# Performance work log

Measured on AMD Instinct MI355X. Metric: run time of the kernel, lower is better.

The kernel has to match this reference:

```python
import jax, jax.numpy as jnp
import numpy as np

N_Q, N_T, D, C = 4096, 8192, 512, 16
SIGMA = 2.0


def setup_inputs() -> dict:
    key = jax.random.key(0)
    k1, k2, k3 = jax.random.split(key, 3)
    X = jax.random.normal(k1, (N_Q, D), dtype=jnp.float32)
    X_train = jax.random.normal(k2, (N_T, D), dtype=jnp.float32)
    y = jax.random.randint(k3, (N_T,), 0, C, dtype=jnp.int32)
    sigma = jnp.float32(SIGMA)
    return {"X": X, "X_train": X_train, "y": y, "sigma": sigma}


def reference(X, X_train, y, sigma):
    xx = jnp.sum(X * X, axis=1, keepdims=True)              # [N_q, 1]
    tt = jnp.sum(X_train * X_train, axis=1)                 # [N_t]
    cross = jnp.einsum('qd,td->qt', X, X_train)             # [N_q, N_t]
    dist2 = jnp.maximum(xx + tt[None, :] - 2.0 * cross, 0.0)
    pattern = jnp.exp(-dist2 / (2.0 * sigma ** 2))          # Gaussian RBF kernel [N_q, N_t]
    # per-class segment sum over training patterns (replaces per-class Python loop)
    summation = jax.ops.segment_sum(pattern.T, y, num_segments=C).T  # [N_q, C]
    summation = summation / jnp.sum(summation, axis=1, keepdims=True)
    return jnp.argmax(summation, axis=1)
```

## Files before the change

kernel.cpp:

```cpp
#include <hip/hip_runtime.h>


#define NQ 4096
#define NT 8192
#define DD 512
#define NC 16
#define LN_FLT_MIN -87.336544750402f
#define SCREEN_T 730.0f

typedef __attribute__((ext_vector_type(4))) int   v4i;
typedef __attribute__((ext_vector_type(8))) int   v8i;
typedef __attribute__((ext_vector_type(16))) float f32x16;

__global__ __launch_bounds__(256) void prep_k(const float* __restrict__ X,
                                              const float* __restrict__ XT,
                                              unsigned char* __restrict__ fXp,
                                              unsigned char* __restrict__ fTp,
                                              float* __restrict__ xx,
                                              float* __restrict__ tt,
                                              float* __restrict__ classacc) {
  const int lane = threadIdx.x & 63;
  const int row  = blockIdx.x * 4 + (threadIdx.x >> 6);
  const float* src; unsigned char* dst; float* nrm; int r;
  if (row < NT) { r = row; src = XT + (size_t)r * DD; dst = fTp; nrm = tt + r; }
  else { r = row - NT; src = X + (size_t)r * DD; dst = fXp; nrm = xx + r; }
  const float4* s4 = (const float4*)src;
  const float4 a = s4[lane * 2], b = s4[lane * 2 + 1];
  int w0 = __builtin_amdgcn_cvt_pk_fp8_f32(a.x, a.y, 0, false);
  w0     = __builtin_amdgcn_cvt_pk_fp8_f32(a.z, a.w, w0, true);
  int w1 = __builtin_amdgcn_cvt_pk_fp8_f32(b.x, b.y, 0, false);
  w1     = __builtin_amdgcn_cvt_pk_fp8_f32(b.z, b.w, w1, true);
  int2 o; o.x = w0; o.y = w1;
  const int l = (r & 31) + 32 * ((lane >> 2) & 1);
  const size_t dest = ((size_t)(r >> 5) * 8 + (lane >> 3)) * 2048
                    + ((lane >> 1) & 1) * 1024 + l * 16 + (lane & 1) * 8;
  *(int2*)(dst + dest) = o;
  float acc = a.x*a.x + a.y*a.y + a.z*a.z + a.w*a.w
            + b.x*b.x + b.y*b.y + b.z*b.z + b.w*b.w;
  #pragma unroll
  for (int off = 32; off; off >>= 1) acc += __shfl_down(acc, off, 64);
  if (lane == 0) *nrm = acc;
  if (blockIdx.x < 64) {
    float4 z = {0.f, 0.f, 0.f, 0.f};
    ((float4*)classacc)[blockIdx.x * 256 + threadIdx.x] = z;
  }
}

#define MFMA(A, B, C) __builtin_amdgcn_mfma_scale_f32_32x32x64_f8f6f4( \
    (A), (B), (C), 0, 0, 0, 127, 0, 127)

static __device__ __forceinline__ v8i ld32(const unsigned char* p) {
  v4i lo = *(const v4i*)p;
  v4i hi = *(const v4i*)(p + 1024);
  return __builtin_shufflevector(lo, hi, 0, 1, 2, 3, 4, 5, 6, 7);
}

__global__ __launch_bounds__(512) void pnn_mfma(const unsigned char* __restrict__ fXp,
                                                const unsigned char* __restrict__ fTp,
                                                const float* __restrict__ Xf,
                                                const float* __restrict__ Tf,
                                                const int* __restrict__ y,
                                                const float* __restrict__ sigp,
                                                const float* __restrict__ xx,
                                                const float* __restrict__ tt,
                                                float* __restrict__ classacc) {
  const int tid  = threadIdx.x;
  const int wid  = tid >> 6, lane = tid & 63;
  const int la   = lane & 31, lb = lane >> 5;
  const int wr   = wid >> 2, wc = wid & 3;

  const int bid = blockIdx.x;
  const int xcd = bid & 7, cc = bid >> 3;
  const int qt  = (xcd & 1) * 16 + (cc >> 3);
  const int tn  = (xcd >> 1) * 8 + (cc & 7);
  const int wq  = qt * 128 + wr * 64;
  const int wt  = tn * 256 + wc * 64;

  const unsigned char* pa = fXp + ((size_t)(wq >> 5) * 8) * 2048 + lane * 16;
  const unsigned char* pb = fTp + ((size_t)(wt >> 5) * 8) * 2048 + lane * 16;

  f32x16 acc00 = (f32x16)(0.f), acc01 = (f32x16)(0.f);
  f32x16 acc10 = (f32x16)(0.f), acc11 = (f32x16)(0.f);

  v8i A0[2], A1[2], B0[2], B1[2];

#define LOADK(s, kt) { \
    A0[s] = ld32(pa + (kt) * 2048); \
    A1[s] = ld32(pa + 16384 + (kt) * 2048); \
    B0[s] = ld32(pb + (kt) * 2048); \
    B1[s] = ld32(pb + 16384 + (kt) * 2048); }

  LOADK(0, 0)
  LOADK(1, 1)
  #pragma unroll
  for (int kt = 0; kt < 8; ++kt) {
    const int s = kt & 1;
    acc00 = MFMA(A0[s], B0[s], acc00);
    acc01 = MFMA(A0[s], B1[s], acc01);
    acc10 = MFMA(A1[s], B0[s], acc10);
    acc11 = MFMA(A1[s], B1[s], acc11);
    if (kt < 6) LOADK(s, kt + 2)
  }
#undef LOADK

  const float sg = sigp[0];
  const float inv2s2 = 1.0f / (2.0f * sg * sg);
  float tnorm[2]; int tcls[2];
  #pragma unroll
  for (int nt = 0; nt < 2; ++nt) {
    const int t = wt + nt * 32 + la;
    tnorm[nt] = tt[t]; tcls[nt] = y[t];
  }

#define EPIL(ACC, mt, nt) { \
    _Pragma("unroll") \
    for (int reg = 0; reg < 16; ++reg) { \
      const int q = wq + (mt) * 32 + (reg & 3) + 8 * (reg >> 2) + 4 * lb; \
      const float xq = xx[q]; \
      const float d2 = xq + tnorm[(nt)] - 2.0f * (ACC)[reg]; \
      if (__builtin_expect(d2 < SCREEN_T, 0)) { \
        const int t = wt + (nt) * 32 + la; \
        const float4* xp = (const float4*)(Xf + (size_t)q * DD); \
        const float4* tp = (const float4*)(Tf + (size_t)t * DD); \
        float s0 = 0.f, s1 = 0.f, s2 = 0.f, s3 = 0.f; \
        for (int d = 0; d < DD / 4; ++d) { \
          const float4 xv = xp[d], tv = tp[d]; \
          s0 = fmaf(xv.x, tv.x, s0); s1 = fmaf(xv.y, tv.y, s1); \
          s2 = fmaf(xv.z, tv.z, s2); s3 = fmaf(xv.w, tv.w, s3); \
        } \
        const float dot = (s0 + s1) + (s2 + s3); \
        const float dd2 = fmaxf(xq + tnorm[(nt)] - 2.0f * dot, 0.f); \
        const float arg = -dd2 * inv2s2; \
        if (arg >= LN_FLT_MIN)             \
          atomicAdd(&classacc[q * NC + tcls[(nt)]], expf(arg)); \
      } \
    } }

  EPIL(acc00, 0, 0)
  EPIL(acc01, 0, 1)
  EPIL(acc10, 1, 0)
  EPIL(acc11, 1, 1)
#undef EPIL
}

__global__ __launch_bounds__(256) void argmax_k(const float* __restrict__ classacc,
                                                float* __restrict__ out) {
  const int q = blockIdx.x * 256 + threadIdx.x;
  float sc[NC];
  #pragma unroll
  for (int c4 = 0; c4 < 4; ++c4) {
    const float4 v = ((const float4*)(classacc + (size_t)q * NC))[c4];
    sc[c4*4+0] = v.x; sc[c4*4+1] = v.y; sc[c4*4+2] = v.z; sc[c4*4+3] = v.w;
  }
  float rowsum = 0.f;
  #pragma unroll
  for (int c = 0; c < NC; ++c) rowsum += sc[c];
  int best = 0; float bv = sc[0];
  #pragma unroll
  for (int c = 1; c < NC; ++c)
    if (sc[c] > bv) { bv = sc[c]; best = c; }
  out[q] = (rowsum > 0.f) ? (float)best : 0.0f;
}

extern "C" void kernel_launch(void* const* d_in, const int* in_sizes, int n_in,
                              void* d_out, int out_size, void* d_ws, size_t ws_size,
                              hipStream_t stream) {
  const float* X  = (const float*)d_in[0];
  const float* XT = (const float*)d_in[1];
  const int*   y  = (const int*)d_in[2];
  const float* sg = (const float*)d_in[3];
  float* out = (float*)d_out;

  char* wsp = (char*)d_ws;
  unsigned char* fXp = (unsigned char*)wsp;
  unsigned char* fTp = fXp + (size_t)NQ * DD;
  float* tt       = (float*)(wsp + 8u * 1024u * 1024u);
  float* xx       = tt + NT;
  float* classacc = xx + NQ;

  prep_k<<<(NQ + NT) / 4, 256, 0, stream>>>(X, XT, fXp, fTp, xx, tt, classacc);
  pnn_mfma<<<1024, 512, 0, stream>>>(fXp, fTp, X, XT, y, sg, xx, tt, classacc);
  argmax_k<<<NQ / 256, 256, 0, stream>>>(classacc, out);
}
```

Measured before the change: 50.85 us.

## Stage FP8 GEMM operand tiles through LDS with async global_load_lds double buffering

Each warp used to load its A/B fragments straight from global memory into registers, with a two-deep register prefetch. Now the block cooperatively copies each K-slice of the shared 128x256 tile into LDS with global_load_lds, double-buffers it, and waits on vmcnt plus barriers before warps read their fragments from LDS. This removes duplicate global loads of operands shared across warps. It also remaps blocks to tiles per XCD for L2 locality and raises MFMA issue priority. The cost is a barrier at every K step and added LDS traffic.

```diff
diff --git a/kernel.cpp b/kernel.cpp
--- a/kernel.cpp
+++ b/kernel.cpp
@@ -48,8 +48,16 @@
 
 #define MFMA(A, B, C) __builtin_amdgcn_mfma_scale_f32_32x32x64_f8f6f4( \
     (A), (B), (C), 0, 0, 0, 127, 0, 127)
-
-static __device__ __forceinline__ v8i ld32(const unsigned char* p) {
+#define BAR() __builtin_amdgcn_s_barrier()
+#define WAITV(N) asm volatile("s_waitcnt vmcnt(" #N ")" ::: "memory")
+
+static __device__ __forceinline__ void gll(const unsigned char* src, char* dst) {
+  __builtin_amdgcn_global_load_lds(
+      (const __attribute__((address_space(1))) unsigned int*)src,
+      (__attribute__((address_space(3))) unsigned int*)dst, 16, 0, 0);
+}
+
+static __device__ __forceinline__ v8i ld32(const char* p) {
   v4i lo = *(const v4i*)p;
   v4i hi = *(const v4i*)(p + 1024);
   return __builtin_shufflevector(lo, hi, 0, 1, 2, 3, 4, 5, 6, 7);
@@ -64,6 +72,7 @@
                                                 const float* __restrict__ xx,
                                                 const float* __restrict__ tt,
                                                 float* __restrict__ classacc) {
+  __shared__ char lds[49152];
   const int tid  = threadIdx.x;
   const int wid  = tid >> 6, lane = tid & 63;
   const int la   = lane & 31, lb = lane >> 5;
@@ -71,38 +80,55 @@
 
   const int bid = blockIdx.x;
   const int xcd = bid & 7, cc = bid >> 3;
-  const int qt  = (xcd & 1) * 16 + (cc >> 3);
-  const int tn  = (xcd >> 1) * 8 + (cc & 7);
-  const int wq  = qt * 128 + wr * 64;
-  const int wt  = tn * 256 + wc * 64;
-
-  const unsigned char* pa = fXp + ((size_t)(wq >> 5) * 8) * 2048 + lane * 16;
-  const unsigned char* pb = fTp + ((size_t)(wt >> 5) * 8) * 2048 + lane * 16;
+  const int qt  = (xcd & 3) * 8 + (cc >> 4);
+  const int tn  = (xcd >> 2) * 16 + (cc & 15);
+  const int qbase = qt * 128, tbase = tn * 256;
+  const int qrt0 = qbase >> 5;
+  const int trt0 = tbase >> 5;
+
+  const int sc = tid >> 7;
+  const int si = (tid & 127) * 16;
+
+#define STAGE(kt, Ab, Bb) { \
+    gll(fXp + ((size_t)(qrt0 + sc) * 8 + (kt)) * 2048 + si, (Ab) + sc * 2048 + si); \
+    gll(fTp + ((size_t)(trt0 + sc) * 8 + (kt)) * 2048 + si, (Bb) + sc * 2048 + si); \
+    gll(fTp + ((size_t)(trt0 + sc + 4) * 8 + (kt)) * 2048 + si, (Bb) + (sc + 4) * 2048 + si); }
+
+  char* const A0 = lds;
+  char* const A1 = lds + 8192;
+  char* const B0 = lds + 16384;
+  char* const B1 = lds + 32768;
 
   f32x16 acc00 = (f32x16)(0.f), acc01 = (f32x16)(0.f);
   f32x16 acc10 = (f32x16)(0.f), acc11 = (f32x16)(0.f);
 
-  v8i A0[2], A1[2], B0[2], B1[2];
-
-#define LOADK(s, kt) { \
-    A0[s] = ld32(pa + (kt) * 2048); \
-    A1[s] = ld32(pa + 16384 + (kt) * 2048); \
-    B0[s] = ld32(pb + (kt) * 2048); \
-    B1[s] = ld32(pb + 16384 + (kt) * 2048); }
-
-  LOADK(0, 0)
-  LOADK(1, 1)
+  STAGE(0, A0, B0)
+
   #pragma unroll
   for (int kt = 0; kt < 8; ++kt) {
-    const int s = kt & 1;
-    acc00 = MFMA(A0[s], B0[s], acc00);
-    acc01 = MFMA(A0[s], B1[s], acc01);
-    acc10 = MFMA(A1[s], B0[s], acc10);
-    acc11 = MFMA(A1[s], B1[s], acc11);
-    if (kt < 6) LOADK(s, kt + 2)
-  }
-#undef LOADK
-
+    char* const Ac = (kt & 1) ? A1 : A0;
+    char* const Bc = (kt & 1) ? B1 : B0;
+    char* const An = (kt & 1) ? A0 : A1;
+    char* const Bn = (kt & 1) ? B0 : B1;
+    if (kt < 7) { STAGE(kt + 1, An, Bn) }
+    if (kt < 7) { WAITV(3); } else { WAITV(0); }
+    BAR();
+    const v8i a0 = ld32(Ac + (wr * 2 + 0) * 2048 + lane * 16);
+    const v8i a1 = ld32(Ac + (wr * 2 + 1) * 2048 + lane * 16);
+    const v8i b0 = ld32(Bc + (wc * 2 + 0) * 2048 + lane * 16);
+    const v8i b1 = ld32(Bc + (wc * 2 + 1) * 2048 + lane * 16);
+    __builtin_amdgcn_s_setprio(1);
+    acc00 = MFMA(a0, b0, acc00);
+    acc01 = MFMA(a0, b1, acc01);
+    acc10 = MFMA(a1, b0, acc10);
+    acc11 = MFMA(a1, b1, acc11);
+    __builtin_amdgcn_s_setprio(0);
+    if (kt < 7) BAR();
+  }
+#undef STAGE
+
+  const int wq = qbase + wr * 64;
+  const int wt = tbase + wc * 64;
   const float sg = sigp[0];
   const float inv2s2 = 1.0f / (2.0f * sg * sg);
   float tnorm[2]; int tcls[2];
```

New measurement: 48.03 us. -5.5%, faster.

## Restructure FP8 GEMM into persistent LDS-staged blocks with triple-buffered async loads

Applied to the files above, without the earlier changes.

The distance GEMM kernel moves from 1024 blocks of 512 threads, each loading its operands straight from global memory into registers, to 256 blocks of 1024 threads. Each block owns 256 queries and a 512-wide training strip and streams A and B tiles into a three-slot LDS ring via global_load_lds, with waitcnt and barrier synchronisation. Query and training norms and labels are cached in LDS, and the screening test is rewritten as a single compare against precomputed half-norms. The epilogue runs every four stages over 128 training columns and then resets the accumulators. This aims to reuse operand tiles across waves and overlap loads with MFMA, at the cost of about 149 KB of LDS per block, one block per CU, and more barrier overhead.

```diff
diff --git a/kernel.cpp b/kernel.cpp
--- a/kernel.cpp
+++ b/kernel.cpp
@@ -48,99 +48,129 @@
 
 #define MFMA(A, B, C) __builtin_amdgcn_mfma_scale_f32_32x32x64_f8f6f4( \
     (A), (B), (C), 0, 0, 0, 127, 0, 127)
-
-static __device__ __forceinline__ v8i ld32(const unsigned char* p) {
+#define BAR() __builtin_amdgcn_s_barrier()
+#define SBAR() __builtin_amdgcn_sched_barrier(0)
+#define WAITV(N) asm volatile("s_waitcnt vmcnt(" #N ")" ::: "memory")
+
+static __device__ __forceinline__ void gll(const void* src, char* dst) {
+  __builtin_amdgcn_global_load_lds(
+      (const __attribute__((address_space(1))) unsigned int*)src,
+      (__attribute__((address_space(3))) unsigned int*)dst, 16, 0, 0);
+}
+
+static __device__ __forceinline__ v8i ld32(const char* p) {
   v4i lo = *(const v4i*)p;
   v4i hi = *(const v4i*)(p + 1024);
   return __builtin_shufflevector(lo, hi, 0, 1, 2, 3, 4, 5, 6, 7);
 }
 
-__global__ __launch_bounds__(512) void pnn_mfma(const unsigned char* __restrict__ fXp,
-                                                const unsigned char* __restrict__ fTp,
-                                                const float* __restrict__ Xf,
-                                                const float* __restrict__ Tf,
-                                                const int* __restrict__ y,
-                                                const float* __restrict__ sigp,
-                                                const float* __restrict__ xx,
-                                                const float* __restrict__ tt,
-                                                float* __restrict__ classacc) {
+__global__ __launch_bounds__(1024) void pnn_mfma(const unsigned char* __restrict__ fXp,
+                                                 const unsigned char* __restrict__ fTp,
+                                                 const float* __restrict__ Xf,
+                                                 const float* __restrict__ Tf,
+                                                 const int* __restrict__ y,
+                                                 const float* __restrict__ sigp,
+                                                 const float* __restrict__ xx,
+                                                 const float* __restrict__ tt,
+                                                 float* __restrict__ classacc) {
+  extern __shared__ char lds[];
+  char*  const Aring = lds;
+  char*  const Bring = lds + 98304;
+  float* const hxs   = (float*)(lds + 147456);
+  float* const tts   = (float*)(lds + 148480);
+  int*   const ycl   = (int*)  (lds + 150528);
+
   const int tid  = threadIdx.x;
-  const int wid  = tid >> 6, lane = tid & 63;
+  const int w    = tid >> 6, lane = tid & 63;
   const int la   = lane & 31, lb = lane >> 5;
-  const int wr   = wid >> 2, wc = wid & 3;
-
-  const int bid = blockIdx.x;
-  const int xcd = bid & 7, cc = bid >> 3;
-  const int qt  = (xcd & 1) * 16 + (cc >> 3);
-  const int tn  = (xcd >> 1) * 8 + (cc & 7);
-  const int wq  = qt * 128 + wr * 64;
-  const int wt  = tn * 256 + wc * 64;
-
-  const unsigned char* pa = fXp + ((size_t)(wq >> 5) * 8) * 2048 + lane * 16;
-  const unsigned char* pb = fTp + ((size_t)(wt >> 5) * 8) * 2048 + lane * 16;
-
-  f32x16 acc00 = (f32x16)(0.f), acc01 = (f32x16)(0.f);
-  f32x16 acc10 = (f32x16)(0.f), acc11 = (f32x16)(0.f);
-
-  v8i A0[2], A1[2], B0[2], B1[2];
-
-#define LOADK(s, kt) { \
-    A0[s] = ld32(pa + (kt) * 2048); \
-    A1[s] = ld32(pa + 16384 + (kt) * 2048); \
-    B0[s] = ld32(pb + (kt) * 2048); \
-    B1[s] = ld32(pb + 16384 + (kt) * 2048); }
-
-  LOADK(0, 0)
-  LOADK(1, 1)
-  #pragma unroll
-  for (int kt = 0; kt < 8; ++kt) {
-    const int s = kt & 1;
-    acc00 = MFMA(A0[s], B0[s], acc00);
-    acc01 = MFMA(A0[s], B1[s], acc01);
-    acc10 = MFMA(A1[s], B0[s], acc10);
-    acc11 = MFMA(A1[s], B1[s], acc11);
-    if (kt < 6) LOADK(s, kt + 2)
-  }
-#undef LOADK
+  const int wr   = w >> 2, wc = w & 3;
+
+  const int bid   = blockIdx.x;
+  const int strip = bid & 15;
+  const int qt    = bid >> 4;
+  const int qbase = qt * 256;
+  const int qrt   = qbase >> 5;
+  const int trt   = strip * 16;
 
   const float sg = sigp[0];
   const float inv2s2 = 1.0f / (2.0f * sg * sg);
-  float tnorm[2]; int tcls[2];
-  #pragma unroll
-  for (int nt = 0; nt < 2; ++nt) {
-    const int t = wt + nt * 32 + la;
-    tnorm[nt] = tt[t]; tcls[nt] = y[t];
-  }
-
-#define EPIL(ACC, mt, nt) { \
+
+#define STAGE(s) { \
+    char* As = Aring + ((s) % 3) * 32768; \
+    char* Bs = Bring + ((s) % 3) * 16384; \
     _Pragma("unroll") \
-    for (int reg = 0; reg < 16; ++reg) { \
-      const int q = wq + (mt) * 32 + (reg & 3) + 8 * (reg >> 2) + 4 * lb; \
-      const float xq = xx[q]; \
-      const float d2 = xq + tnorm[(nt)] - 2.0f * (ACC)[reg]; \
-      if (__builtin_expect(d2 < SCREEN_T, 0)) { \
-        const int t = wt + (nt) * 32 + la; \
-        const float4* xp = (const float4*)(Xf + (size_t)q * DD); \
-        const float4* tp = (const float4*)(Tf + (size_t)t * DD); \
-        float s0 = 0.f, s1 = 0.f, s2 = 0.f, s3 = 0.f; \
-        for (int d = 0; d < DD / 4; ++d) { \
-          const float4 xv = xp[d], tv = tp[d]; \
-          s0 = fmaf(xv.x, tv.x, s0); s1 = fmaf(xv.y, tv.y, s1); \
-          s2 = fmaf(xv.z, tv.z, s2); s3 = fmaf(xv.w, tv.w, s3); \
+    for (int j = 0; j < 2; ++j) { \
+      const int L = j * 16384 + tid * 16; \
+      const int c = L >> 11, o = L & 2047; \
+      gll(fXp + ((size_t)(qrt + (c >> 1)) * 8 + ((s) & 3) * 2 + (c & 1)) * 2048 + o, As + L); \
+    } \
+    { const int L = tid * 16; \
+      const int c = L >> 11, o = L & 2047; \
+      gll(fTp + ((size_t)(trt + ((s) >> 2) * 4 + (c >> 1)) * 8 + ((s) & 3) * 2 + (c & 1)) * 2048 + o, Bs + L); } \
+  }
+
+  STAGE(0)
+  STAGE(1)
+  float xv = 0.f, tv = 0.f; int yv = 0;
+  if (tid < 256) xv = xx[qbase + tid];
+  if (tid < 512) { tv = tt[strip * 512 + tid]; yv = y[strip * 512 + tid]; }
+  if (tid < 256) hxs[tid] = (xv - SCREEN_T) * 0.5f;
+  if (tid < 512) { tts[tid] = tv * 0.5f; ycl[tid] = yv; }
+  __syncthreads();
+
+  f32x16 acc0 = (f32x16)(0.f), acc1 = (f32x16)(0.f);
+
+  #pragma unroll
+  for (int s = 0; s < 16; ++s) {
+    if (s <= 14) { WAITV(3); } else { WAITV(0); }
+    SBAR();
+    BAR();
+    if (s <= 13) STAGE(s + 2)
+    const char* As = Aring + (s % 3) * 32768;
+    const char* Bs = Bring + (s % 3) * 16384;
+    #pragma unroll
+    for (int ktp = 0; ktp < 2; ++ktp) {
+      const v8i a0 = ld32(As + (((wr * 2 + 0) * 2) + ktp) * 2048 + lane * 16);
+      const v8i a1 = ld32(As + (((wr * 2 + 1) * 2) + ktp) * 2048 + lane * 16);
+      const v8i b  = ld32(Bs + ((wc * 2) + ktp) * 2048 + lane * 16);
+      acc0 = MFMA(a0, b, acc0);
+      acc1 = MFMA(a1, b, acc1);
+    }
+
+    if ((s & 3) == 3) {
+      const int T = s >> 2;
+      const int tloc = T * 128 + wc * 32 + la;
+      const float tn = tts[tloc];
+#define EPIL(ACC, mt) { \
+      _Pragma("unroll") \
+      for (int reg = 0; reg < 16; ++reg) { \
+        const int ql = wr * 64 + (mt) * 32 + (reg & 3) + 8 * (reg >> 2) + 4 * lb; \
+        if (__builtin_expect((ACC)[reg] > hxs[ql] + tn, 0)) { \
+          const int q  = qbase + ql; \
+          const int tg = strip * 512 + tloc; \
+          const float4* xp = (const float4*)(Xf + (size_t)q * DD); \
+          const float4* tp = (const float4*)(Tf + (size_t)tg * DD); \
+          float s0 = 0.f, s1 = 0.f, s2 = 0.f, s3 = 0.f; \
+          for (int d = 0; d < DD / 4; ++d) { \
+            const float4 xw = xp[d], tw = tp[d]; \
+            s0 = fmaf(xw.x, tw.x, s0); s1 = fmaf(xw.y, tw.y, s1); \
+            s2 = fmaf(xw.z, tw.z, s2); s3 = fmaf(xw.w, tw.w, s3); \
+          } \
+          const float dot = (s0 + s1) + (s2 + s3); \
+          const float dd2 = fmaxf(xx[q] + tt[tg] - 2.0f * dot, 0.f); \
+          const float arg = -dd2 * inv2s2; \
+          if (arg >= LN_FLT_MIN)           \
+            atomicAdd(&classacc[q * NC + ycl[tloc]], expf(arg)); \
         } \
-        const float dot = (s0 + s1) + (s2 + s3); \
-        const float dd2 = fmaxf(xq + tnorm[(nt)] - 2.0f * dot, 0.f); \
-        const float arg = -dd2 * inv2s2; \
-        if (arg >= LN_FLT_MIN)             \
-          atomicAdd(&classacc[q * NC + tcls[(nt)]], expf(arg)); \
-      } \
-    } }
-
-  EPIL(acc00, 0, 0)
-  EPIL(acc01, 0, 1)
-  EPIL(acc10, 1, 0)
-  EPIL(acc11, 1, 1)
+      } }
+      EPIL(acc0, 0)
+      EPIL(acc1, 1)
 #undef EPIL
+      acc0 = (f32x16)(0.f);
+      acc1 = (f32x16)(0.f);
+    }
+  }
+#undef STAGE
 }
 
 __global__ __launch_bounds__(256) void argmax_k(const float* __restrict__ classacc,
@@ -178,7 +208,10 @@
   float* xx       = tt + NT;
   float* classacc = xx + NQ;
 
+  (void)hipFuncSetAttribute((const void*)pnn_mfma,
+                            hipFuncAttributeMaxDynamicSharedMemorySize, 152576);
+
   prep_k<<<(NQ + NT) / 4, 256, 0, stream>>>(X, XT, fXp, fTp, xx, tt, classacc);
-  pnn_mfma<<<1024, 512, 0, stream>>>(fXp, fTp, X, XT, y, sg, xx, tt, classacc);
+  pnn_mfma<<<256, 1024, 152576, stream>>>(fXp, fTp, X, XT, y, sg, xx, tt, classacc);
   argmax_k<<<NQ / 256, 256, 0, stream>>>(classacc, out);
 }
```

After: 167.6 us. 3.3x slower.
